# Kernel tuning notes

Hardware: AMD Instinct MI355X
Metric: run time of the kernel (lower is better)

Reference implementation:

```python
import jax, jax.numpy as jnp
import numpy as np
from jax.scipy.special import logsumexp

N, T, F, S, L = 16, 800, 90, 128, 200
NEG = -1e30
DEN_SCALE = 1.0


def setup_inputs() -> dict:
    key = jax.random.key(0)
    ks = jax.random.split(key, 6)
    # nnet_output is the output of log_softmax (per the docstring)
    logits = jax.random.normal(ks[0], (N, T, F), dtype=jnp.float32)
    nnet_output = jax.nn.log_softmax(logits, axis=-1)
    seq_idx = jnp.arange(N, dtype=jnp.int32)
    starts = jnp.zeros((N,), dtype=jnp.int32)
    nframes = jax.random.randint(ks[1], (N,), T // 2, T + 1).astype(jnp.int32)
    supervision_segments = jnp.stack([seq_idx, starts, nframes], axis=1)
    # shared denominator graph: dense log transition weights + state phone labels
    den_trans = jax.random.normal(ks[2], (S, S), dtype=jnp.float32) - 2.0
    den_labels = jax.random.randint(ks[3], (S,), 0, F).astype(jnp.int32)
    # numerator linear-chain graphs: per-utterance phone label sequences
    num_labels = jax.random.randint(ks[4], (N, L), 0, F).astype(jnp.int32)
    num_lens = jax.random.randint(ks[5], (N,), L // 2, L + 1).astype(jnp.int32)
    return {
        'nnet_output': nnet_output,
        'supervision_segments': supervision_segments,
        'den_trans': den_trans,
        'den_labels': den_labels,
        'num_labels': num_labels,
        'num_lens': num_lens,
    }


def _mmi_tot_scores(nnet_output, num_frames, den_trans, den_labels, num_labels, num_lens):
    """Log-semiring forward scores: num - den_scale * den per utterance."""
    x = jnp.transpose(nnet_output, (1, 0, 2))  # [T, N, F]
    ts = jnp.arange(T)

    # ---- denominator: shared dense WFSA, forward algorithm ----
    def den_step(alpha, inp):
        x_t, t = inp  # x_t: [N, F]
        emit = x_t[:, den_labels]  # [N, S] gather of frame log-probs
        new = logsumexp(alpha[:, :, None] + den_trans[None, :, :], axis=1) + emit
        alpha = jnp.where((t < num_frames)[:, None], new, alpha)
        return alpha, None

    a0 = jnp.full((N, S), NEG, dtype=nnet_output.dtype).at[:, 0].set(0.0)
    den_alpha, _ = jax.lax.scan(den_step, a0, (x, ts))
    den_scores = logsumexp(den_alpha, axis=1)  # [N]

    # ---- numerator: per-utterance linear chain (self-loop or advance) ----
    def num_step(alpha, inp):
        x_t, t = inp
        emit = jnp.take_along_axis(x_t, num_labels, axis=1)  # [N, L]
        body = jnp.logaddexp(alpha[:, 1:], alpha[:, :L]) + emit
        new = jnp.concatenate(
            [jnp.full((N, 1), NEG, dtype=alpha.dtype), body], axis=1)
        alpha = jnp.where((t < num_frames)[:, None], new, alpha)
        return alpha, None

    b0 = jnp.full((N, L + 1), NEG, dtype=nnet_output.dtype).at[:, 0].set(0.0)
    num_alpha, _ = jax.lax.scan(num_step, b0, (x, ts))
    num_scores = jnp.take_along_axis(num_alpha, num_lens[:, None], axis=1)[:, 0]

    return num_scores - DEN_SCALE * den_scores


def reference(nnet_output, supervision_segments, den_trans, den_labels, num_labels, num_lens):
    num_frames = supervision_segments[:, 2]
    tot = _mmi_tot_scores(nnet_output, num_frames, den_trans, den_labels,
                          num_labels, num_lens)
    # drop sequences whose score diverged (mirrors get_tot_objf_and_num_frames)
    finite = jnp.isfinite(tot) & (tot > 0.5 * NEG)
    tot_score = jnp.sum(jnp.where(finite, tot, 0.0))
    tot_frames = jnp.sum(jnp.where(finite, num_frames, 0))
    all_frames = jnp.sum(num_frames)
    return tot_score, tot_frames, all_frames
```

## Files before the change

kernel.cpp:

```cpp
#include <hip/hip_runtime.h>
#include <math.h>

#define NB 16
#define TT 800
#define FF 90
#define SS 128
#define LL 200
#define NEGV (-1e30f)

#define DNODES 16
#define DNDRX 50
#define QNODES 32
#define QDRX 25
#define BROW 26
#define NEGH (-60000.0f)
#define RST 68
#define LN2F 0.69314718055994531f
#define LOG2E 1.4426950408889634f

typedef __attribute__((ext_vector_type(8))) short short8;
typedef __attribute__((ext_vector_type(4))) float float4v;

static __device__ __forceinline__ unsigned short f2bf(float x) {
    union { float f; unsigned u; } v; v.f = x;
    unsigned r = (v.u + 0x7FFFu + ((v.u >> 16) & 1u)) >> 16;
    return (unsigned short)r;
}
static __device__ __forceinline__ unsigned pack2bf_t(float a, float b) {
    return (__float_as_uint(a) >> 16) | (__float_as_uint(b) & 0xFFFF0000u);
}

__global__ __launch_bounds__(256) void mmi_prep(const float* __restrict__ trans,
                                                unsigned* __restrict__ AF) {
    const int idx = blockIdx.x * 256 + threadIdx.x;
    const int l  = idx & 63, fk = idx >> 6;
    const int mt = fk >> 2, kc = fk & 3;
    const int q  = l >> 4,  m15 = l & 15;
    unsigned wv[4];
    #pragma unroll
    for (int j2 = 0; j2 < 4; ++j2) {
        const float a = __expf(trans[(kc * 32 + q * 8 + 2 * j2    ) * SS + mt * 16 + m15]);
        const float b = __expf(trans[(kc * 32 + q * 8 + 2 * j2 + 1) * SS + mt * 16 + m15]);
        wv[j2] = (unsigned)f2bf(a) | ((unsigned)f2bf(b) << 16);
    }
    *(uint4*)(AF + 4 * idx) = make_uint4(wv[0], wv[1], wv[2], wv[3]);
}

__global__ __launch_bounds__(512, 2) void mmi_nodes(
    const float* __restrict__ x,
    const int*   __restrict__ sup,
    const float* __restrict__ trans,
    const int*   __restrict__ den_labels,
    const int*   __restrict__ num_labels,
    const unsigned* __restrict__ AF,
    unsigned*    __restrict__ Pout,
    float*       __restrict__ scales8,
    _Float16*    __restrict__ Bd)
{
    __shared__ __align__(16) unsigned char SMEM[60448];
    const int tid = threadIdx.x;

    if (blockIdx.x < NB * DNODES) {
        unsigned* Xs  = (unsigned*)SMEM;
        float* ptab   = (float*)(SMEM + 34816);

        const int bid = blockIdx.x;
        const int u  = bid >> 4;
        const int nd = bid & 15;
        const int t0 = nd * DNDRX;
        const int nf = sup[u * 3 + 2];
        unsigned* Pg = Pout + (size_t)bid * 8192;

        if (t0 >= nf) {
            #pragma unroll
            for (int k2 = 0; k2 < 16; ++k2) {
                const int ww = tid + k2 * 512;
                const int row = ww >> 6, colw = ww & 63;
                unsigned val = 0;
                if (row == 2 * colw)     val |= 0x3F80u;
                if (row == 2 * colw + 1) val |= 0x3F800000u;
                Pg[ww] = val;
            }
            if (tid < 8) scales8[bid * 8 + tid] = 0.0f;
            return;
        }

        const int w = tid >> 6, l = tid & 63;
        const int m15 = l & 15, q = l >> 4;

        for (int idx = tid; idx < DNDRX * SS; idx += 512) {
            const int tt = idx >> 7, d = idx & 127;
            const int fr = min(t0 + tt, TT - 1);
            ptab[idx] = __expf(x[((size_t)u * TT + fr) * FF + den_labels[d]]);
        }
        __syncthreads();

        unsigned* Xw = Xs + w * (16 * RST);
        {
            const float p0 = ptab[2 * l], p1 = ptab[2 * l + 1];
            #pragma unroll
            for (int k2 = 0; k2 < 16; ++k2) {
                const int R = w * 16 + k2;
                const float2 t2 = ((const float2*)trans)[R * 64 + l];
                Xw[k2 * RST + l] = pack2bf_t(__expf(t2.x) * p0, __expf(t2.y) * p1);
            }
        }

        short8 afrag[8][4];
        #pragma unroll
        for (int mt = 0; mt < 8; ++mt)
            #pragma unroll
            for (int kc = 0; kc < 4; ++kc)
                afrag[mt][kc] = *(const short8*)(AF + ((mt * 4 + kc) * 64 + l) * 4);

        const unsigned short* XwH = (const unsigned short*)Xw;
        const int kmax = min(DNDRX, nf - t0);
        int eacc = 0;
        float redmax = 1.0f;

        for (int k = 1; k < kmax; ++k) {
            float sc = 1.0f;
            if ((k & 3) == 0) {
                const float mm = fmaxf(redmax, 1e-37f);
                const int e = (int)((__float_as_uint(mm) >> 23) & 255u);
                sc = __uint_as_float((unsigned)(254 - e) << 23);
                eacc += (e - 127);
            }

            short8 bf[4];
            #pragma unroll
            for (int kc = 0; kc < 4; ++kc)
                bf[kc] = *(const short8*)(XwH + m15 * (2 * RST) + kc * 32 + q * 8);

            float4v acc[8];
            #pragma unroll
            for (int mt = 0; mt < 8; ++mt) {
                float4v z = {0.f, 0.f, 0.f, 0.f};
                acc[mt] = z;
            }
            #pragma unroll
            for (int kc = 0; kc < 4; ++kc)
                #pragma unroll
                for (int mt = 0; mt < 8; ++mt)
                    acc[mt] = __builtin_amdgcn_mfma_f32_16x16x32_bf16(
                        afrag[mt][kc], bf[kc], acc[mt], 0, 0, 0);

            const bool dmax = ((k & 3) == 3);
            float vmax = 0.0f;
            #pragma unroll
            for (int mt = 0; mt < 8; ++mt) {
                float4 pc = *(const float4*)(ptab + k * SS + mt * 16 + 4 * q);
                pc.x *= sc; pc.y *= sc; pc.z *= sc; pc.w *= sc;
                acc[mt][0] *= pc.x;
                acc[mt][1] *= pc.y;
                acc[mt][2] *= pc.z;
                acc[mt][3] *= pc.w;
                if (dmax)
                    vmax = fmaxf(vmax,
                        fmaxf(fmaxf(acc[mt][0], acc[mt][1]),
                              fmaxf(acc[mt][2], acc[mt][3])));
            }
            if (dmax) {
                #pragma unroll
                for (int off = 32; off >= 1; off >>= 1)
                    vmax = fmaxf(vmax, __shfl_xor(vmax, off, 64));
                redmax = vmax;
            }

            #pragma unroll
            for (int mt = 0; mt < 8; ++mt) {
                uint2 pk;
                pk.x = pack2bf_t(acc[mt][0], acc[mt][1]);
                pk.y = pack2bf_t(acc[mt][2], acc[mt][3]);
                *(uint2*)(Xw + m15 * RST + mt * 8 + 2 * q) = pk;
            }
        }

        #pragma unroll
        for (int k2 = 0; k2 < 16; ++k2)
            Pg[(w * 16 + k2) * 64 + l] = Xw[k2 * RST + l];
        if (l == 0) scales8[bid * 8 + w] = (float)eacc;
        return;
    }

    {
        float* est = (float*)SMEM;

        const int qb    = blockIdx.x - NB * DNODES;
        const int slot0 = qb * 2;
        const int u     = slot0 / QNODES;
        const int nd0   = slot0 - u * QNODES;
        const int nf    = sup[u * 3 + 2];
        const int* nlu  = num_labels + u * LL;

        for (int idx = tid; idx < 2 * QDRX * 200; idx += 512) {
            const int g   = idx / (QDRX * 200);
            const int rem = idx - g * (QDRX * 200);
            const int tt  = rem / 200;
            const int j   = rem - tt * 200;
            const int fr  = min((nd0 + g) * QDRX + tt, TT - 1);
            est[idx] = x[((size_t)u * TT + fr) * FF + nlu[j]] * LOG2E;
        }
        __syncthreads();

        const int g  = tid >> 8;
        const int c  = tid & 255;
        const int nd = nd0 + g;
        const int t0 = nd * QDRX;
        const int kmaxg = min(QDRX, max(nf - t0, 0));
        const float* eg = est + g * (QDRX * 200);

        float a[BROW];
        a[0] = 0.0f;
        #pragma unroll
        for (int d = 1; d < BROW; ++d) a[d] = NEGV;

        for (int t = 0; t < kmaxg; ++t) {
            const float* et = eg + t * 200;
            #pragma unroll
            for (int d = BROW - 1; d >= 1; --d) {
                const float e  = et[min(c + d - 1, 199)];
                const float aa = a[d], bb = a[d - 1];
                const float mx = fmaxf(aa, bb);
                const float dd = fminf(aa, bb) - mx;
                a[d] = e + mx +
                       __builtin_amdgcn_logf(1.0f + __builtin_amdgcn_exp2f(dd));
            }
            a[0] = (c == 0) ? NEGV : (et[min(c - 1, 199)] + a[0]);
        }

        if (c <= 200) {
            _Float16* Bg = Bd + (size_t)(slot0 + g) * 201 * BROW;
            #pragma unroll
            for (int d = 0; d < BROW; ++d) {
                const int r = c + d;
                if (r <= 200) Bg[r * BROW + d] = (_Float16)fmaxf(a[d], NEGH);
            }
            if (c < BROW - 1) {
                for (int kk = c + 1; kk < BROW; ++kk)
                    Bg[c * BROW + kk] = (_Float16)NEGH;
            }
        }
    }
}

__global__ __launch_bounds__(256) void mmi_chain(
    const unsigned short* __restrict__ Pmat,
    const _Float16* __restrict__ Bd,
    const float* __restrict__ scales8,
    const int* __restrict__ num_lens,
    float* __restrict__ dsc)
{
    __shared__ float sh_v[SS];
    __shared__ float sh_part[8 * SS];
    __shared__ float sh_red[2];
    __shared__ float ab[2][232];

    const int tid = threadIdx.x;

    if (blockIdx.x < NB) {
        const int u = blockIdx.x;
        const int gg = tid & 31, c = tid >> 5;
        const unsigned short* Pu = Pmat + (size_t)u * DNODES * 16384;

        if (tid < SS) sh_v[tid] = (tid == 0) ? 1.0f : 0.0f;
        int   e2acc = 0;
        float sscal = 0.0f;

        uint2 curm[16], nxt[16];
        #pragma unroll
        for (int j = 0; j < 16; ++j)
            curm[j] = *(const uint2*)(Pu + (16 * c + j) * SS + 4 * gg);
        __syncthreads();

        for (int i = 0; i < DNODES; ++i) {
            if (i + 1 < DNODES) {
                const unsigned short* Pn = Pu + (size_t)(i + 1) * 16384;
                #pragma unroll
                for (int j = 0; j < 16; ++j)
                    nxt[j] = *(const uint2*)(Pn + (16 * c + j) * SS + 4 * gg);
            }
            const float* s8 = scales8 + (size_t)(u * DNODES + i) * 8;
            float gmax = s8[0];
            #pragma unroll
            for (int g2 = 1; g2 < 8; ++g2) gmax = fmaxf(gmax, s8[g2]);
            const float fgr = __builtin_amdgcn_exp2f(s8[c] - gmax);
            sscal += gmax;

            const float4* av = (const float4*)(sh_v + 16 * c);
            float4 aa[4] = {av[0], av[1], av[2], av[3]};
            const float* as = (const float*)aa;
            float4 acc = make_float4(0.f, 0.f, 0.f, 0.f);
            #pragma unroll
            for (int j = 0; j < 16; ++j) {
                const float e0 = __uint_as_float(curm[j].x << 16);
                const float e1 = __uint_as_float(curm[j].x & 0xFFFF0000u);
                const float e2 = __uint_as_float(curm[j].y << 16);
                const float e3 = __uint_as_float(curm[j].y & 0xFFFF0000u);
                acc.x = fmaf(as[j], e0, acc.x);
                acc.y = fmaf(as[j], e1, acc.y);
                acc.z = fmaf(as[j], e2, acc.z);
                acc.w = fmaf(as[j], e3, acc.w);
            }
            acc.x *= fgr; acc.y *= fgr; acc.z *= fgr; acc.w *= fgr;
            *(float4*)(sh_part + c * SS + 4 * gg) = acc;
            __syncthreads();

            float v = 0.0f;
            if (tid < SS) {
                float y = 0.0f;
                #pragma unroll
                for (int cc = 0; cc < 8; ++cc) y += sh_part[cc * SS + tid];
                v = y;
                float m = v;
                #pragma unroll
                for (int off = 32; off >= 1; off >>= 1)
                    m = fmaxf(m, __shfl_xor(m, off, 64));
                if ((tid & 63) == 0) sh_red[tid >> 6] = m;
            }
            __syncthreads();
            if (tid < SS) {
                const float mm = fmaxf(fmaxf(sh_red[0], sh_red[1]), 1e-37f);
                const int e = (int)((__float_as_uint(mm) >> 23) & 255u);
                const float inv = __uint_as_float((unsigned)(254 - e) << 23);
                e2acc += (e - 127);
                sh_v[tid] = v * inv;
            }
            #pragma unroll
            for (int j = 0; j < 16; ++j) curm[j] = nxt[j];
            __syncthreads();
        }

        if (tid < SS) {
            float s = sh_v[tid];
            #pragma unroll
            for (int off = 32; off >= 1; off >>= 1)
                s += __shfl_xor(s, off, 64);
            if ((tid & 63) == 0) sh_red[tid >> 6] = s;
        }
        __syncthreads();
        if (tid == 0)
            dsc[u] = LN2F * ((float)e2acc + sscal) + __logf(sh_red[0] + sh_red[1]);
    } else {
        const int u = blockIdx.x - NB;
        const _Float16* Bu = Bd + (size_t)u * QNODES * 201 * BROW;
        const int r = tid;

        if (r < 232) { ab[0][r] = NEGV; ab[1][r] = NEGV; }
        float dv[BROW];
        if (r < 201) {
            #pragma unroll
            for (int k = 0; k < BROW; ++k) dv[k] = (float)Bu[r * BROW + k];
        }
        __syncthreads();
        if (r == 0) ab[0][QDRX] = 0.0f;
        __syncthreads();

        int cur = 0;
        for (int nd = 0; nd < QNODES; ++nd) {
            _Float16 nx[BROW];
            if (nd + 1 < QNODES && r < 201) {
                const _Float16* src = Bu + ((size_t)(nd + 1) * 201 + r) * BROW;
                #pragma unroll
                for (int k = 0; k < BROW; ++k) nx[k] = src[k];
            }
            float anew = NEGV;
            if (r < 201) {
                float tr[BROW];
                #pragma unroll
                for (int k = 0; k < BROW; ++k)
                    tr[k] = dv[k] + ab[cur][QDRX + r - k];
                float m = tr[0];
                #pragma unroll
                for (int k = 1; k < BROW; ++k) m = fmaxf(m, tr[k]);
                float s = 0.0f;
                #pragma unroll
                for (int k = 0; k < BROW; ++k)
                    s += __builtin_amdgcn_exp2f(tr[k] - m);
                anew = m + __builtin_amdgcn_logf(s);
            }
            if (r < 201) ab[cur ^ 1][QDRX + r] = anew;
            cur ^= 1;
            __syncthreads();
            if (r < 201) {
                #pragma unroll
                for (int k = 0; k < BROW; ++k) dv[k] = (float)nx[k];
            }
        }
        if (r == 0) dsc[NB + u] = ab[cur][QDRX + num_lens[u]] * LN2F;
    }
}

__global__ void mmi_finalize(const float* __restrict__ sc,
                             const int* __restrict__ sup,
                             float* __restrict__ out)
{
    const int tid = threadIdx.x;
    float tot_score = 0.0f, tot_frames = 0.0f, all_frames = 0.0f;
    if (tid < NB) {
        const float tot = sc[NB + tid] - sc[tid];
        const int nf = sup[tid * 3 + 2];
        const bool fin = isfinite(tot) && (tot > 0.5f * NEGV);
        tot_score  = fin ? tot : 0.0f;
        tot_frames = fin ? (float)nf : 0.0f;
        all_frames = (float)nf;
    }
    #pragma unroll
    for (int off = 32; off >= 1; off >>= 1) {
        tot_score  += __shfl_xor(tot_score, off, 64);
        tot_frames += __shfl_xor(tot_frames, off, 64);
        all_frames += __shfl_xor(all_frames, off, 64);
    }
    if (tid == 0) {
        out[0] = tot_score;
        out[1] = tot_frames;
        out[2] = all_frames;
    }
}

#define XBF (16 * FF)
__global__ __launch_bounds__(256) void mmi_forward_fb(
    const float* __restrict__ x, const int* __restrict__ sup,
    const float* __restrict__ trans, const int* __restrict__ den_labels,
    const int* __restrict__ num_labels, const int* __restrict__ num_lens,
    float* __restrict__ ws)
{
    const int tid = threadIdx.x;
    if (blockIdx.x < NB) {
        __shared__ float sh_v[SS];
        __shared__ float sh_part[8 * SS];
        __shared__ float sh_red[4];
        __shared__ __align__(16) float xbuf[2][XBF];
        const int n = blockIdx.x, nf = sup[n * 3 + 2];
        const int g = tid & 31, c = tid >> 5;
        float4 e[16];
        #pragma unroll
        for (int j = 0; j < 16; ++j) {
            const float4 t4 = *(const float4*)(trans + (size_t)(16 * c + j) * SS + 4 * g);
            e[j] = make_float4(__expf(t4.x), __expf(t4.y), __expf(t4.z), __expf(t4.w));
        }
        const int lab = (tid < SS) ? den_labels[tid & (SS - 1)] : 0;
        const float* xb = x + (size_t)n * TT * FF;
        {
            const float4* s0 = (const float4*)xb;
            float4 p0 = s0[tid]; float4 p1; if (tid < 104) p1 = s0[256 + tid];
            float4* d0 = (float4*)xbuf[0];
            d0[tid] = p0; if (tid < 104) d0[256 + tid] = p1;
        }
        if (tid < SS) sh_v[tid] = (tid == 0) ? 1.0f : 0.0f;
        float logM = 0.0f, v = 0.0f, pe = 0.0f;
        float4 pf0, pf1;
        __syncthreads();
        for (int t = 0; t < nf; ++t) {
            const int b = t >> 4;
            if (tid < SS) pe = __expf(xbuf[b & 1][(t & 15) * FF + lab]);
            float4 aa[4];
            { const float4* av = (const float4*)(sh_v + 16 * c);
              aa[0] = av[0]; aa[1] = av[1]; aa[2] = av[2]; aa[3] = av[3]; }
            const float* as = (const float*)aa;
            float4 acc = make_float4(0.f, 0.f, 0.f, 0.f);
            #pragma unroll
            for (int j = 0; j < 16; ++j) {
                acc.x = fmaf(as[j], e[j].x, acc.x); acc.y = fmaf(as[j], e[j].y, acc.y);
                acc.z = fmaf(as[j], e[j].z, acc.z); acc.w = fmaf(as[j], e[j].w, acc.w);
            }
            *(float4*)(sh_part + c * SS + 4 * g) = acc;
            if ((t & 15) == 8) {
                const int tn = (b + 1) * 16;
                if (tn < nf) {
                    const float4* s = (const float4*)(xb + (size_t)tn * FF);
                    pf0 = s[tid]; if (tid < 104) pf1 = s[256 + tid];
                }
            }
            __syncthreads();
            const bool rs = ((t & 15) == 15);
            if (tid < SS) {
                float y = 0.0f;
                #pragma unroll
                for (int cc = 0; cc < 8; ++cc) y += sh_part[cc * SS + tid];
                v = y * pe;
                if (rs) {
                    float m = v;
                    #pragma unroll
                    for (int off = 32; off >= 1; off >>= 1)
                        m = fmaxf(m, __shfl_xor(m, off, 64));
                    if ((tid & 63) == 0) sh_red[tid >> 6] = m;
                }
            }
            if (rs) {
                const int tn = (b + 1) * 16;
                if (tn < nf) {
                    float4* dst = (float4*)xbuf[(b + 1) & 1];
                    dst[tid] = pf0; if (tid < 104) dst[256 + tid] = pf1;
                }
                __syncthreads();
                if (tid < SS) {
                    float mm = fmaxf(fmaxf(sh_red[0], sh_red[1]), 1e-37f);
                    v *= (1.0f / mm); logM += __logf(mm);
                }
            }
            if (tid < SS) sh_v[tid] = v;
            __syncthreads();
        }
        if (tid < SS) {
            float ssum = v;
            #pragma unroll
            for (int off = 32; off >= 1; off >>= 1) ssum += __shfl_xor(ssum, off, 64);
            if ((tid & 63) == 0) sh_red[2 + (tid >> 6)] = ssum;
        }
        __syncthreads();
        if (tid == 0) ws[n] = logM + __logf(sh_red[2] + sh_red[3]);
    } else {
        const int w = tid >> 6, l = tid & 63;
        const int n = (blockIdx.x - NB) * 4 + w;
        const int nf = sup[n * 3 + 2];
        const float* xb = x + (size_t)n * TT * FF;
        const int* nl = num_labels + n * LL;
        int li[4];
        #pragma unroll
        for (int k = 0; k < 4; ++k) li[k] = nl[min(4 * l + k, LL - 1)];
        float a4[4] = {NEGV, NEGV, NEGV, NEGV};
        float ea[4], eb[4];
        #pragma unroll
        for (int k = 0; k < 4; ++k) ea[k] = xb[li[k]];
        { const float* xr = xb + (size_t)min(1, nf - 1) * FF;
          #pragma unroll
          for (int k = 0; k < 4; ++k) eb[k] = xr[li[k]]; }
        auto step = [&](float (&ee)[4], int t) {
            float left = __shfl_up(a4[3], 1, 64);
            if (l == 0) left = (t == 0) ? 0.0f : NEGV;
            float prev = left;
            #pragma unroll
            for (int k = 0; k < 4; ++k) {
                const float a = a4[k], b = prev;
                const float mx = fmaxf(a, b), mn = fminf(a, b);
                const float nv = mx + __logf(1.0f + __expf(mn - mx)) + ee[k];
                prev = a4[k]; a4[k] = nv;
            }
            const int t2 = min(t + 2, nf - 1);
            const float* xr = xb + (size_t)t2 * FF;
            #pragma unroll
            for (int k = 0; k < 4; ++k) ee[k] = xr[li[k]];
        };
        int t = 0;
        while (t < nf) { step(ea, t); ++t; if (t >= nf) break; step(eb, t); ++t; }
        const int idx = num_lens[n] - 1;
        if ((idx >> 2) == l) {
            const int kk = idx & 3;
            float vv = (kk == 0) ? a4[0] : (kk == 1) ? a4[1] : (kk == 2) ? a4[2] : a4[3];
            ws[NB + n] = vv;
        }
    }
}

extern "C" void kernel_launch(void* const* d_in, const int* in_sizes, int n_in,
                              void* d_out, int out_size, void* d_ws, size_t ws_size,
                              hipStream_t stream) {
    const float* x          = (const float*)d_in[0];
    const int*   sup        = (const int*)d_in[1];
    const float* trans      = (const float*)d_in[2];
    const int*   den_labels = (const int*)d_in[3];
    const int*   num_labels = (const int*)d_in[4];
    const int*   num_lens   = (const int*)d_in[5];
    float* out = (float*)d_out;

    const size_t PBYTES = (size_t)NB * DNODES * 32768;
    const size_t BBYTES = (size_t)NB * QNODES * 201 * BROW * 2;
    const size_t SCB    = (size_t)NB * DNODES * 8 * sizeof(float);
    const size_t SOFF   = PBYTES + BBYTES;
    const size_t AOFF   = SOFF + SCB + 64 * sizeof(float);
    const size_t NEEDED = AOFF + 2048 * 16;

    if (ws_size >= NEEDED) {
        unsigned*  Pout    = (unsigned*)d_ws;
        _Float16*  Bd      = (_Float16*)((char*)d_ws + PBYTES);
        float*     scales8 = (float*)((char*)d_ws + SOFF);
        float*     scores  = scales8 + NB * DNODES * 8;
        unsigned*  AF      = (unsigned*)((char*)d_ws + AOFF);
        mmi_prep<<<dim3(8), dim3(256), 0, stream>>>(trans, AF);
        mmi_nodes<<<dim3(512), dim3(512), 0, stream>>>(
            x, sup, trans, den_labels, num_labels, AF, Pout, scales8, Bd);
        mmi_chain<<<dim3(2 * NB), dim3(256), 0, stream>>>(
            (const unsigned short*)d_ws, Bd, scales8, num_lens, scores);
        mmi_finalize<<<dim3(1), dim3(64), 0, stream>>>(scores, sup, out);
    } else {
        float* ws = (float*)d_ws;
        mmi_forward_fb<<<dim3(20), dim3(256), 0, stream>>>(
            x, sup, trans, den_labels, num_labels, num_lens, ws);
        mmi_finalize<<<dim3(1), dim3(64), 0, stream>>>(ws, sup, out);
    }
}
```

Before: 188.1 us.

## Fuse prep, node, chain and finalize kernels via last-block atomic counters

Merges the four launches into one kernel. Each block now builds the bf16 transition fragments itself in shared memory, and per-utterance atomic counters let the last node block of each utterance run the chain reduction. A final counter then lets one block do the finalize. This removes three kernel launches and the gaps between them, in exchange for redundant fragment setup in every block, a memset launch, and serialized chain work inside the tail blocks. The bf16 pack is also switched to a byte-permute instruction, and the emission table gets padded rows.

Measured after the change: 359.8 us. +91.3%, slower.

```diff
diff --git a/kernel.cpp b/kernel.cpp
--- a/kernel.cpp
+++ b/kernel.cpp
@@ -15,6 +15,7 @@
 #define BROW 26
 #define NEGH (-60000.0f)
 #define RST 68
+#define EPAD 228
 #define LN2F 0.69314718055994531f
 #define LOG2E 1.4426950408889634f
 
@@ -26,46 +27,33 @@
     unsigned r = (v.u + 0x7FFFu + ((v.u >> 16) & 1u)) >> 16;
     return (unsigned short)r;
 }
-static __device__ __forceinline__ unsigned pack2bf_t(float a, float b) {
-    return (__float_as_uint(a) >> 16) | (__float_as_uint(b) & 0xFFFF0000u);
+static __device__ __forceinline__ unsigned packperm(float a, float b) {
+    return __builtin_amdgcn_perm(__float_as_uint(b), __float_as_uint(a),
+                                 0x07060302u);
 }
 
-__global__ __launch_bounds__(256) void mmi_prep(const float* __restrict__ trans,
-                                                unsigned* __restrict__ AF) {
-    const int idx = blockIdx.x * 256 + threadIdx.x;
-    const int l  = idx & 63, fk = idx >> 6;
-    const int mt = fk >> 2, kc = fk & 3;
-    const int q  = l >> 4,  m15 = l & 15;
-    unsigned wv[4];
-    #pragma unroll
-    for (int j2 = 0; j2 < 4; ++j2) {
-        const float a = __expf(trans[(kc * 32 + q * 8 + 2 * j2    ) * SS + mt * 16 + m15]);
-        const float b = __expf(trans[(kc * 32 + q * 8 + 2 * j2 + 1) * SS + mt * 16 + m15]);
-        wv[j2] = (unsigned)f2bf(a) | ((unsigned)f2bf(b) << 16);
-    }
-    *(uint4*)(AF + 4 * idx) = make_uint4(wv[0], wv[1], wv[2], wv[3]);
-}
-
-__global__ __launch_bounds__(512, 2) void mmi_nodes(
+__global__ __launch_bounds__(512, 2) void mmi_all(
     const float* __restrict__ x,
     const int*   __restrict__ sup,
     const float* __restrict__ trans,
     const int*   __restrict__ den_labels,
     const int*   __restrict__ num_labels,
-    const unsigned* __restrict__ AF,
+    const int*   __restrict__ num_lens,
     unsigned*    __restrict__ Pout,
     float*       __restrict__ scales8,
-    _Float16*    __restrict__ Bd)
+    _Float16*    __restrict__ Bd,
+    float*       __restrict__ dsc,
+    int*         __restrict__ ctr,
+    float*       __restrict__ out)
 {
     __shared__ __align__(16) unsigned char SMEM[60448];
+    __shared__ int sflag;
     const int tid = threadIdx.x;
+    int u;
 
     if (blockIdx.x < NB * DNODES) {
-        unsigned* Xs  = (unsigned*)SMEM;
-        float* ptab   = (float*)(SMEM + 34816);
-
         const int bid = blockIdx.x;
-        const int u  = bid >> 4;
+        u = bid >> 4;
         const int nd = bid & 15;
         const int t0 = nd * DNDRX;
         const int nf = sup[u * 3 + 2];
@@ -82,312 +70,376 @@
                 Pg[ww] = val;
             }
             if (tid < 8) scales8[bid * 8 + tid] = 0.0f;
-            return;
-        }
-
-        const int w = tid >> 6, l = tid & 63;
-        const int m15 = l & 15, q = l >> 4;
-
-        for (int idx = tid; idx < DNDRX * SS; idx += 512) {
-            const int tt = idx >> 7, d = idx & 127;
-            const int fr = min(t0 + tt, TT - 1);
-            ptab[idx] = __expf(x[((size_t)u * TT + fr) * FF + den_labels[d]]);
-        }
+        } else {
+            unsigned* AFs = (unsigned*)SMEM;
+            const int w = tid >> 6, l = tid & 63;
+            const int m15 = l & 15, q = l >> 4;
+
+            #pragma unroll
+            for (int i = 0; i < 16; ++i) {
+                const int wi = tid + i * 512;
+                const int f  = wi >> 2, j2 = wi & 3;
+                const int fl = f & 63, kc = (f >> 6) & 3, mt = f >> 8;
+                const int col = mt * 16 + (fl & 15);
+                const int krow = kc * 32 + (fl >> 4) * 8 + 2 * j2;
+                const float a = __expf(trans[(krow    ) * SS + col]);
+                const float b = __expf(trans[(krow + 1) * SS + col]);
+                AFs[wi] = (unsigned)f2bf(a) | ((unsigned)f2bf(b) << 16);
+            }
+            __syncthreads();
+            short8 afrag[8][4];
+            #pragma unroll
+            for (int mt = 0; mt < 8; ++mt)
+                #pragma unroll
+                for (int kc = 0; kc < 4; ++kc)
+                    afrag[mt][kc] =
+                        *(const short8*)(AFs + ((mt * 4 + kc) * 64 + l) * 4);
+            __syncthreads();
+
+            unsigned* Xs  = (unsigned*)SMEM;
+            float* ptab   = (float*)(SMEM + 34816);
+
+            for (int idx = tid; idx < DNDRX * SS; idx += 512) {
+                const int tt = idx >> 7, d = idx & 127;
+                const int fr = min(t0 + tt, TT - 1);
+                ptab[idx] = __expf(x[((size_t)u * TT + fr) * FF + den_labels[d]]);
+            }
+            __syncthreads();
+
+            unsigned* Xw = Xs + w * (16 * RST);
+            {
+                const float p0 = ptab[2 * l], p1 = ptab[2 * l + 1];
+                #pragma unroll
+                for (int k2 = 0; k2 < 16; ++k2) {
+                    const int R = w * 16 + k2;
+                    const float2 t2 = ((const float2*)trans)[R * 64 + l];
+                    Xw[k2 * RST + l] = packperm(__expf(t2.x) * p0,
+                                                __expf(t2.y) * p1);
+                }
+            }
+
+            const unsigned short* XwH = (const unsigned short*)Xw;
+            const int kmax = min(DNDRX, nf - t0);
+            int eacc = 0;
+            float redmax = 1.0f;
+
+            for (int k = 1; k < kmax; ++k) {
+                const bool dosc = ((k & 3) == 0);
+                float sc = 1.0f;
+                if (dosc) {
+                    const float mm = fmaxf(redmax, 1e-37f);
+                    const int e = (int)((__float_as_uint(mm) >> 23) & 255u);
+                    sc = __uint_as_float((unsigned)(254 - e) << 23);
+                    eacc += (e - 127);
+                }
+
+                short8 bf[4];
+                #pragma unroll
+                for (int kc = 0; kc < 4; ++kc)
+                    bf[kc] = *(const short8*)(XwH + m15 * (2 * RST) +
+                                              kc * 32 + q * 8);
+
+                float4v acc[8];
+                #pragma unroll
+                for (int mt = 0; mt < 8; ++mt) {
+                    float4v z = {0.f, 0.f, 0.f, 0.f};
+                    acc[mt] = z;
+                }
+                #pragma unroll
+                for (int kc = 0; kc < 4; ++kc)
+                    #pragma unroll
+                    for (int mt = 0; mt < 8; ++mt)
+                        acc[mt] = __builtin_amdgcn_mfma_f32_16x16x32_bf16(
+                            afrag[mt][kc], bf[kc], acc[mt], 0, 0, 0);
+
+                const bool dmax = ((k & 3) == 3);
+                float vmax = 0.0f;
+                #pragma unroll
+                for (int mt = 0; mt < 8; ++mt) {
+                    float4 pc = *(const float4*)(ptab + k * SS + mt * 16 + 4 * q);
+                    if (dosc) { pc.x *= sc; pc.y *= sc; pc.z *= sc; pc.w *= sc; }
+                    acc[mt][0] *= pc.x;
+                    acc[mt][1] *= pc.y;
+                    acc[mt][2] *= pc.z;
+                    acc[mt][3] *= pc.w;
+                    if (dmax)
+                        vmax = fmaxf(vmax,
+                            fmaxf(fmaxf(acc[mt][0], acc[mt][1]),
+                                  fmaxf(acc[mt][2], acc[mt][3])));
+                }
+                if (dmax) {
+                    #pragma unroll
+                    for (int off = 32; off >= 1; off >>= 1)
+                        vmax = fmaxf(vmax, __shfl_xor(vmax, off, 64));
+                    redmax = vmax;
+                }
+
+                #pragma unroll
+                for (int mt = 0; mt < 8; ++mt) {
+                    uint2 pk;
+                    pk.x = packperm(acc[mt][0], acc[mt][1]);
+                    pk.y = packperm(acc[mt][2], acc[mt][3]);
+                    *(uint2*)(Xw + m15 * RST + mt * 8 + 2 * q) = pk;
+                }
+            }
+
+            #pragma unroll
+            for (int k2 = 0; k2 < 16; ++k2)
+                Pg[(w * 16 + k2) * 64 + l] = Xw[k2 * RST + l];
+            if (l == 0) scales8[bid * 8 + w] = (float)eacc;
+        }
+
+        __threadfence();
+        if (tid == 0) sflag = (atomicAdd(&ctr[u], 1) == DNODES - 1);
         __syncthreads();
-
-        unsigned* Xw = Xs + w * (16 * RST);
+        if (!sflag) return;
         {
-            const float p0 = ptab[2 * l], p1 = ptab[2 * l + 1];
-            #pragma unroll
-            for (int k2 = 0; k2 < 16; ++k2) {
-                const int R = w * 16 + k2;
-                const float2 t2 = ((const float2*)trans)[R * 64 + l];
-                Xw[k2 * RST + l] = pack2bf_t(__expf(t2.x) * p0, __expf(t2.y) * p1);
-            }
-        }
-
-        short8 afrag[8][4];
-        #pragma unroll
-        for (int mt = 0; mt < 8; ++mt)
-            #pragma unroll
-            for (int kc = 0; kc < 4; ++kc)
-                afrag[mt][kc] = *(const short8*)(AF + ((mt * 4 + kc) * 64 + l) * 4);
-
-        const unsigned short* XwH = (const unsigned short*)Xw;
-        const int kmax = min(DNDRX, nf - t0);
-        int eacc = 0;
-        float redmax = 1.0f;
-
-        for (int k = 1; k < kmax; ++k) {
-            float sc = 1.0f;
-            if ((k & 3) == 0) {
-                const float mm = fmaxf(redmax, 1e-37f);
-                const int e = (int)((__float_as_uint(mm) >> 23) & 255u);
-                sc = __uint_as_float((unsigned)(254 - e) << 23);
-                eacc += (e - 127);
-            }
-
-            short8 bf[4];
-            #pragma unroll
-            for (int kc = 0; kc < 4; ++kc)
-                bf[kc] = *(const short8*)(XwH + m15 * (2 * RST) + kc * 32 + q * 8);
-
-            float4v acc[8];
-            #pragma unroll
-            for (int mt = 0; mt < 8; ++mt) {
-                float4v z = {0.f, 0.f, 0.f, 0.f};
-                acc[mt] = z;
-            }
-            #pragma unroll
-            for (int kc = 0; kc < 4; ++kc)
-                #pragma unroll
-                for (int mt = 0; mt < 8; ++mt)
-                    acc[mt] = __builtin_amdgcn_mfma_f32_16x16x32_bf16(
-                        afrag[mt][kc], bf[kc], acc[mt], 0, 0, 0);
-
-            const bool dmax = ((k & 3) == 3);
-            float vmax = 0.0f;
-            #pragma unroll
-            for (int mt = 0; mt < 8; ++mt) {
-                float4 pc = *(const float4*)(ptab + k * SS + mt * 16 + 4 * q);
-                pc.x *= sc; pc.y *= sc; pc.z *= sc; pc.w *= sc;
-                acc[mt][0] *= pc.x;
-                acc[mt][1] *= pc.y;
-                acc[mt][2] *= pc.z;
-                acc[mt][3] *= pc.w;
-                if (dmax)
-                    vmax = fmaxf(vmax,
-                        fmaxf(fmaxf(acc[mt][0], acc[mt][1]),
-                              fmaxf(acc[mt][2], acc[mt][3])));
-            }
-            if (dmax) {
+            float* sh_v    = (float*)SMEM;
+            float* sh_part = (float*)(SMEM + 512);
+            float* sh_red  = (float*)(SMEM + 4608);
+            __syncthreads();
+
+            const bool act = tid < 256;
+            const int gg = tid & 31, c = tid >> 5;
+            const unsigned short* Pu =
+                (const unsigned short*)(Pout + (size_t)u * DNODES * 8192);
+
+            if (tid < SS) sh_v[tid] = (tid == 0) ? 1.0f : 0.0f;
+            int   e2acc = 0;
+            float sscal = 0.0f;
+
+            uint2 curm[16], nxt[16];
+            if (act) {
+                #pragma unroll
+                for (int j = 0; j < 16; ++j)
+                    curm[j] = *(const uint2*)(Pu + (16 * c + j) * SS + 4 * gg);
+            }
+            __syncthreads();
+
+            for (int i = 0; i < DNODES; ++i) {
+                if (act && i + 1 < DNODES) {
+                    const unsigned short* Pn = Pu + (size_t)(i + 1) * 16384;
+                    #pragma unroll
+                    for (int j = 0; j < 16; ++j)
+                        nxt[j] = *(const uint2*)(Pn + (16 * c + j) * SS + 4 * gg);
+                }
+                float fgr = 0.0f;
+                if (act) {
+                    const float* s8 = scales8 + (size_t)(u * DNODES + i) * 8;
+                    float gmax = s8[0];
+                    #pragma unroll
+                    for (int g2 = 1; g2 < 8; ++g2) gmax = fmaxf(gmax, s8[g2]);
+                    fgr = __builtin_amdgcn_exp2f(s8[c & 7] - gmax);
+                    sscal += gmax;
+                }
+                if (act) {
+                    const float4* av = (const float4*)(sh_v + 16 * c);
+                    float4 aa[4] = {av[0], av[1], av[2], av[3]};
+                    const float* as = (const float*)aa;
+                    float4 acc = make_float4(0.f, 0.f, 0.f, 0.f);
+                    #pragma unroll
+                    for (int j = 0; j < 16; ++j) {
+                        const float e0 = __uint_as_float(curm[j].x << 16);
+                        const float e1 = __uint_as_float(curm[j].x & 0xFFFF0000u);
+                        const float e2 = __uint_as_float(curm[j].y << 16);
+                        const float e3 = __uint_as_float(curm[j].y & 0xFFFF0000u);
+                        acc.x = fmaf(as[j], e0, acc.x);
+                        acc.y = fmaf(as[j], e1, acc.y);
+                        acc.z = fmaf(as[j], e2, acc.z);
+                        acc.w = fmaf(as[j], e3, acc.w);
+                    }
+                    acc.x *= fgr; acc.y *= fgr; acc.z *= fgr; acc.w *= fgr;
+                    *(float4*)(sh_part + c * SS + 4 * gg) = acc;
+                }
+                __syncthreads();
+
+                float v = 0.0f;
+                if (tid < SS) {
+                    float y = 0.0f;
+                    #pragma unroll
+                    for (int cc = 0; cc < 8; ++cc) y += sh_part[cc * SS + tid];
+                    v = y;
+                    float m = v;
+                    #pragma unroll
+                    for (int off = 32; off >= 1; off >>= 1)
+                        m = fmaxf(m, __shfl_xor(m, off, 64));
+                    if ((tid & 63) == 0) sh_red[tid >> 6] = m;
+                }
+                __syncthreads();
+                if (tid < SS) {
+                    const float mm = fmaxf(fmaxf(sh_red[0], sh_red[1]), 1e-37f);
+                    const int e = (int)((__float_as_uint(mm) >> 23) & 255u);
+                    const float inv = __uint_as_float((unsigned)(254 - e) << 23);
+                    e2acc += (e - 127);
+                    sh_v[tid] = v * inv;
+                }
+                if (act) {
+                    #pragma unroll
+                    for (int j = 0; j < 16; ++j) curm[j] = nxt[j];
+                }
+                __syncthreads();
+            }
+
+            if (tid < SS) {
+                float s = sh_v[tid];
                 #pragma unroll
                 for (int off = 32; off >= 1; off >>= 1)
-                    vmax = fmaxf(vmax, __shfl_xor(vmax, off, 64));
-                redmax = vmax;
-            }
-
-            #pragma unroll
-            for (int mt = 0; mt < 8; ++mt) {
-                uint2 pk;
-                pk.x = pack2bf_t(acc[mt][0], acc[mt][1]);
-                pk.y = pack2bf_t(acc[mt][2], acc[mt][3]);
-                *(uint2*)(Xw + m15 * RST + mt * 8 + 2 * q) = pk;
-            }
-        }
-
-        #pragma unroll
-        for (int k2 = 0; k2 < 16; ++k2)
-            Pg[(w * 16 + k2) * 64 + l] = Xw[k2 * RST + l];
-        if (l == 0) scales8[bid * 8 + w] = (float)eacc;
-        return;
-    }
-
-    {
-        float* est = (float*)SMEM;
+                    s += __shfl_xor(s, off, 64);
+                if ((tid & 63) == 0) sh_red[tid >> 6] = s;
+            }
+            __syncthreads();
+            if (tid == 0)
+                dsc[u] = LN2F * ((float)e2acc + sscal) +
+                         __logf(sh_red[0] + sh_red[1]);
+        }
+    } else {
+        float* est = (float*)(SMEM + 16);
 
         const int qb    = blockIdx.x - NB * DNODES;
         const int slot0 = qb * 2;
-        const int u     = slot0 / QNODES;
+        u = slot0 / QNODES;
         const int nd0   = slot0 - u * QNODES;
         const int nf    = sup[u * 3 + 2];
         const int* nlu  = num_labels + u * LL;
 
-        for (int idx = tid; idx < 2 * QDRX * 200; idx += 512) {
-            const int g   = idx / (QDRX * 200);
-            const int rem = idx - g * (QDRX * 200);
-            const int tt  = rem / 200;
-            const int j   = rem - tt * 200;
+        for (int idx = tid; idx < 2 * QDRX * EPAD; idx += 512) {
+            const int g   = idx / (QDRX * EPAD);
+            const int rem = idx - g * (QDRX * EPAD);
+            const int tt  = rem / EPAD;
+            const int j   = rem - tt * EPAD;
+            const int jj  = min(j, 199);
             const int fr  = min((nd0 + g) * QDRX + tt, TT - 1);
-            est[idx] = x[((size_t)u * TT + fr) * FF + nlu[j]] * LOG2E;
+            est[idx] = x[((size_t)u * TT + fr) * FF + nlu[jj]] * LOG2E;
         }
         __syncthreads();
 
-        const int g  = tid >> 8;
-        const int c  = tid & 255;
-        const int nd = nd0 + g;
-        const int t0 = nd * QDRX;
-        const int kmaxg = min(QDRX, max(nf - t0, 0));
-        const float* eg = est + g * (QDRX * 200);
-
-        float a[BROW];
-        a[0] = 0.0f;
+        {
+            const int g  = tid >> 8;
+            const int c  = tid & 255;
+            const int nd = nd0 + g;
+            const int t0 = nd * QDRX;
+            const int kmaxg = min(QDRX, max(nf - t0, 0));
+            const float* eg = est + g * (QDRX * EPAD);
+
+            float a[BROW];
+            a[0] = 0.0f;
+            #pragma unroll
+            for (int d = 1; d < BROW; ++d) a[d] = NEGV;
+
+            const float* etc = eg + (c - 1);
+            for (int t = 0; t < kmaxg; ++t, etc += EPAD) {
+                const int tc = t + 1;
+                #pragma unroll
+                for (int d = BROW - 1; d >= 1; --d) {
+                    if (d <= tc) {
+                        const float e  = etc[d];
+                        const float aa = a[d], bb = a[d - 1];
+                        const float mx = fmaxf(aa, bb);
+                        const float dd = fminf(aa, bb) - mx;
+                        a[d] = e + mx +
+                            __builtin_amdgcn_logf(
+                                1.0f + __builtin_amdgcn_exp2f(dd));
+                    }
+                }
+                a[0] = (c == 0) ? NEGV : (etc[0] + a[0]);
+            }
+
+            if (c <= 200) {
+                _Float16* Bg = Bd + (size_t)(slot0 + g) * 201 * BROW;
+                #pragma unroll
+                for (int d = 0; d < BROW; ++d) {
+                    const int r = c + d;
+                    if (r <= 200) Bg[r * BROW + d] = (_Float16)fmaxf(a[d], NEGH);
+                }
+                if (c < BROW - 1) {
+                    for (int kk = c + 1; kk < BROW; ++kk)
+                        Bg[c * BROW + kk] = (_Float16)NEGH;
+                }
+            }
+        }
+
+        __threadfence();
+        if (tid == 0) sflag = (atomicAdd(&ctr[NB + u], 1) == QNODES / 2 - 1);
+        __syncthreads();
+        if (!sflag) return;
+        {
+            float (*ab)[232] = (float (*)[232])SMEM;
+            __syncthreads();
+
+            const _Float16* Bu = Bd + (size_t)u * QNODES * 201 * BROW;
+            const int r = tid;
+
+            if (r < 232) { ab[0][r] = NEGV; ab[1][r] = NEGV; }
+            float dv[BROW];
+            if (r < 201) {
+                #pragma unroll
+                for (int k = 0; k < BROW; ++k) dv[k] = (float)Bu[r * BROW + k];
+            }
+            __syncthreads();
+            if (r == 0) ab[0][QDRX] = 0.0f;
+            __syncthreads();
+
+            int cur = 0;
+            for (int nd = 0; nd < QNODES; ++nd) {
+                _Float16 nx[BROW];
+                if (nd + 1 < QNODES && r < 201) {
+                    const _Float16* src = Bu + ((size_t)(nd + 1) * 201 + r) * BROW;
+                    #pragma unroll
+                    for (int k = 0; k < BROW; ++k) nx[k] = src[k];
+                }
+                float anew = NEGV;
+                if (r < 201) {
+                    float tr[BROW];
+                    #pragma unroll
+                    for (int k = 0; k < BROW; ++k)
+                        tr[k] = dv[k] + ab[cur][QDRX + r - k];
+                    float m = tr[0];
+                    #pragma unroll
+                    for (int k = 1; k < BROW; ++k) m = fmaxf(m, tr[k]);
+                    float s = 0.0f;
+                    #pragma unroll
+                    for (int k = 0; k < BROW; ++k)
+                        s += __builtin_amdgcn_exp2f(tr[k] - m);
+                    anew = m + __builtin_amdgcn_logf(s);
+                }
+                if (r < 201) ab[cur ^ 1][QDRX + r] = anew;
+                cur ^= 1;
+                __syncthreads();
+                if (r < 201) {
+                    #pragma unroll
+                    for (int k = 0; k < BROW; ++k) dv[k] = (float)nx[k];
+                }
+            }
+            if (r == 0) dsc[NB + u] = ab[cur][QDRX + num_lens[u]] * LN2F;
+        }
+    }
+
+    __threadfence();
+    if (tid == 0) sflag = (atomicAdd(&ctr[2 * NB], 1) == 2 * NB - 1);
+    __syncthreads();
+    if (!sflag) return;
+    __threadfence();
+    if (tid < 64) {
+        float tot_score = 0.0f, tot_frames = 0.0f, all_frames = 0.0f;
+        if (tid < NB) {
+            const float tot = dsc[NB + tid] - dsc[tid];
+            const int nf = sup[tid * 3 + 2];
+            const bool fin = isfinite(tot) && (tot > 0.5f * NEGV);
+            tot_score  = fin ? tot : 0.0f;
+            tot_frames = fin ? (float)nf : 0.0f;
+            all_frames = (float)nf;
+        }
         #pragma unroll
-        for (int d = 1; d < BROW; ++d) a[d] = NEGV;
-
-        for (int t = 0; t < kmaxg; ++t) {
-            const float* et = eg + t * 200;
-            #pragma unroll
-            for (int d = BROW - 1; d >= 1; --d) {
-                const float e  = et[min(c + d - 1, 199)];
-                const float aa = a[d], bb = a[d - 1];
-                const float mx = fmaxf(aa, bb);
-                const float dd = fminf(aa, bb) - mx;
-                a[d] = e + mx +
-                       __builtin_amdgcn_logf(1.0f + __builtin_amdgcn_exp2f(dd));
-            }
-            a[0] = (c == 0) ? NEGV : (et[min(c - 1, 199)] + a[0]);
-        }
-
-        if (c <= 200) {
-            _Float16* Bg = Bd + (size_t)(slot0 + g) * 201 * BROW;
-            #pragma unroll
-            for (int d = 0; d < BROW; ++d) {
-                const int r = c + d;
-                if (r <= 200) Bg[r * BROW + d] = (_Float16)fmaxf(a[d], NEGH);
-            }
-            if (c < BROW - 1) {
-                for (int kk = c + 1; kk < BROW; ++kk)
-                    Bg[c * BROW + kk] = (_Float16)NEGH;
-            }
-        }
-    }
-}
-
-__global__ __launch_bounds__(256) void mmi_chain(
-    const unsigned short* __restrict__ Pmat,
-    const _Float16* __restrict__ Bd,
-    const float* __restrict__ scales8,
-    const int* __restrict__ num_lens,
-    float* __restrict__ dsc)
-{
-    __shared__ float sh_v[SS];
-    __shared__ float sh_part[8 * SS];
-    __shared__ float sh_red[2];
-    __shared__ float ab[2][232];
-
-    const int tid = threadIdx.x;
-
-    if (blockIdx.x < NB) {
-        const int u = blockIdx.x;
-        const int gg = tid & 31, c = tid >> 5;
-        const unsigned short* Pu = Pmat + (size_t)u * DNODES * 16384;
-
-        if (tid < SS) sh_v[tid] = (tid == 0) ? 1.0f : 0.0f;
-        int   e2acc = 0;
-        float sscal = 0.0f;
-
-        uint2 curm[16], nxt[16];
-        #pragma unroll
-        for (int j = 0; j < 16; ++j)
-            curm[j] = *(const uint2*)(Pu + (16 * c + j) * SS + 4 * gg);
-        __syncthreads();
-
-        for (int i = 0; i < DNODES; ++i) {
-            if (i + 1 < DNODES) {
-                const unsigned short* Pn = Pu + (size_t)(i + 1) * 16384;
-                #pragma unroll
-                for (int j = 0; j < 16; ++j)
-                    nxt[j] = *(const uint2*)(Pn + (16 * c + j) * SS + 4 * gg);
-            }
-            const float* s8 = scales8 + (size_t)(u * DNODES + i) * 8;
-            float gmax = s8[0];
-            #pragma unroll
-            for (int g2 = 1; g2 < 8; ++g2) gmax = fmaxf(gmax, s8[g2]);
-            const float fgr = __builtin_amdgcn_exp2f(s8[c] - gmax);
-            sscal += gmax;
-
-            const float4* av = (const float4*)(sh_v + 16 * c);
-            float4 aa[4] = {av[0], av[1], av[2], av[3]};
-            const float* as = (const float*)aa;
-            float4 acc = make_float4(0.f, 0.f, 0.f, 0.f);
-            #pragma unroll
-            for (int j = 0; j < 16; ++j) {
-                const float e0 = __uint_as_float(curm[j].x << 16);
-                const float e1 = __uint_as_float(curm[j].x & 0xFFFF0000u);
-                const float e2 = __uint_as_float(curm[j].y << 16);
-                const float e3 = __uint_as_float(curm[j].y & 0xFFFF0000u);
-                acc.x = fmaf(as[j], e0, acc.x);
-                acc.y = fmaf(as[j], e1, acc.y);
-                acc.z = fmaf(as[j], e2, acc.z);
-                acc.w = fmaf(as[j], e3, acc.w);
-            }
-            acc.x *= fgr; acc.y *= fgr; acc.z *= fgr; acc.w *= fgr;
-            *(float4*)(sh_part + c * SS + 4 * gg) = acc;
-            __syncthreads();
-
-            float v = 0.0f;
-            if (tid < SS) {
-                float y = 0.0f;
-                #pragma unroll
-                for (int cc = 0; cc < 8; ++cc) y += sh_part[cc * SS + tid];
-                v = y;
-                float m = v;
-                #pragma unroll
-                for (int off = 32; off >= 1; off >>= 1)
-                    m = fmaxf(m, __shfl_xor(m, off, 64));
-                if ((tid & 63) == 0) sh_red[tid >> 6] = m;
-            }
-            __syncthreads();
-            if (tid < SS) {
-                const float mm = fmaxf(fmaxf(sh_red[0], sh_red[1]), 1e-37f);
-                const int e = (int)((__float_as_uint(mm) >> 23) & 255u);
-                const float inv = __uint_as_float((unsigned)(254 - e) << 23);
-                e2acc += (e - 127);
-                sh_v[tid] = v * inv;
-            }
-            #pragma unroll
-            for (int j = 0; j < 16; ++j) curm[j] = nxt[j];
-            __syncthreads();
-        }
-
-        if (tid < SS) {
-            float s = sh_v[tid];
-            #pragma unroll
-            for (int off = 32; off >= 1; off >>= 1)
-                s += __shfl_xor(s, off, 64);
-            if ((tid & 63) == 0) sh_red[tid >> 6] = s;
-        }
-        __syncthreads();
-        if (tid == 0)
-            dsc[u] = LN2F * ((float)e2acc + sscal) + __logf(sh_red[0] + sh_red[1]);
-    } else {
-        const int u = blockIdx.x - NB;
-        const _Float16* Bu = Bd + (size_t)u * QNODES * 201 * BROW;
-        const int r = tid;
-
-        if (r < 232) { ab[0][r] = NEGV; ab[1][r] = NEGV; }
-        float dv[BROW];
-        if (r < 201) {
-            #pragma unroll
-            for (int k = 0; k < BROW; ++k) dv[k] = (float)Bu[r * BROW + k];
-        }
-        __syncthreads();
-        if (r == 0) ab[0][QDRX] = 0.0f;
-        __syncthreads();
-
-        int cur = 0;
-        for (int nd = 0; nd < QNODES; ++nd) {
-            _Float16 nx[BROW];
-            if (nd + 1 < QNODES && r < 201) {
-                const _Float16* src = Bu + ((size_t)(nd + 1) * 201 + r) * BROW;
-                #pragma unroll
-                for (int k = 0; k < BROW; ++k) nx[k] = src[k];
-            }
-            float anew = NEGV;
-            if (r < 201) {
-                float tr[BROW];
-                #pragma unroll
-                for (int k = 0; k < BROW; ++k)
-                    tr[k] = dv[k] + ab[cur][QDRX + r - k];
-                float m = tr[0];
-                #pragma unroll
-                for (int k = 1; k < BROW; ++k) m = fmaxf(m, tr[k]);
-                float s = 0.0f;
-                #pragma unroll
-                for (int k = 0; k < BROW; ++k)
-                    s += __builtin_amdgcn_exp2f(tr[k] - m);
-                anew = m + __builtin_amdgcn_logf(s);
-            }
-            if (r < 201) ab[cur ^ 1][QDRX + r] = anew;
-            cur ^= 1;
-            __syncthreads();
-            if (r < 201) {
-                #pragma unroll
-                for (int k = 0; k < BROW; ++k) dv[k] = (float)nx[k];
-            }
-        }
-        if (r == 0) dsc[NB + u] = ab[cur][QDRX + num_lens[u]] * LN2F;
+        for (int off = 32; off >= 1; off >>= 1) {
+            tot_score  += __shfl_xor(tot_score, off, 64);
+            tot_frames += __shfl_xor(tot_frames, off, 64);
+            all_frames += __shfl_xor(all_frames, off, 64);
+        }
+        if (tid == 0) {
+            out[0] = tot_score;
+            out[1] = tot_frames;
+            out[2] = all_frames;
+        }
     }
 }
 
@@ -568,21 +620,20 @@
     const size_t BBYTES = (size_t)NB * QNODES * 201 * BROW * 2;
     const size_t SCB    = (size_t)NB * DNODES * 8 * sizeof(float);
     const size_t SOFF   = PBYTES + BBYTES;
-    const size_t AOFF   = SOFF + SCB + 64 * sizeof(float);
-    const size_t NEEDED = AOFF + 2048 * 16;
+    const size_t DOFF   = SOFF + SCB;
+    const size_t COFF   = DOFF + 256;
+    const size_t NEEDED = COFF + 256;
 
     if (ws_size >= NEEDED) {
         unsigned*  Pout    = (unsigned*)d_ws;
         _Float16*  Bd      = (_Float16*)((char*)d_ws + PBYTES);
         float*     scales8 = (float*)((char*)d_ws + SOFF);
-        float*     scores  = scales8 + NB * DNODES * 8;
-        unsigned*  AF      = (unsigned*)((char*)d_ws + AOFF);
-        mmi_prep<<<dim3(8), dim3(256), 0, stream>>>(trans, AF);
-        mmi_nodes<<<dim3(512), dim3(512), 0, stream>>>(
-            x, sup, trans, den_labels, num_labels, AF, Pout, scales8, Bd);
-        mmi_chain<<<dim3(2 * NB), dim3(256), 0, stream>>>(
-            (const unsigned short*)d_ws, Bd, scales8, num_lens, scores);
-        mmi_finalize<<<dim3(1), dim3(64), 0, stream>>>(scores, sup, out);
+        float*     dsc     = (float*)((char*)d_ws + DOFF);
+        int*       ctr     = (int*)((char*)d_ws + COFF);
+        hipMemsetAsync(ctr, 0, 256, stream);
+        mmi_all<<<dim3(512), dim3(512), 0, stream>>>(
+            x, sup, trans, den_labels, num_labels, num_lens,
+            Pout, scales8, Bd, dsc, ctr, out);
     } else {
         float* ws = (float*)d_ws;
         mmi_forward_fb<<<dim3(20), dim3(256), 0, stream>>>(
```

## Halve den ptab in two phases, pad numerator emission rows, skip unreachable diagonals

Applied to the files above, without the earlier changes.

The denominator node path now computes the emission-probability table in two 25-frame phases instead of one 50-frame table. This shrinks shared memory from about 60KB to 47KB, presumably to allow more resident blocks, at the cost of an extra barrier and a mid-loop reload. The numerator path pads emission rows to 228 so per-element min() clamps disappear, and it skips diagonals d greater than t+1, which cannot yet hold finite values. The bf16 packing now uses a byte-permute instruction, and the scale multiply is applied only on rescale steps.

Result: faster. 183.0 us (-2.7%).

```diff
diff --git a/kernel.cpp b/kernel.cpp
--- a/kernel.cpp
+++ b/kernel.cpp
@@ -10,11 +10,13 @@
 
 #define DNODES 16
 #define DNDRX 50
+#define PTROWS 25
 #define QNODES 32
 #define QDRX 25
 #define BROW 26
 #define NEGH (-60000.0f)
 #define RST 68
+#define EPAD 228
 #define LN2F 0.69314718055994531f
 #define LOG2E 1.4426950408889634f
 
@@ -26,8 +28,9 @@
     unsigned r = (v.u + 0x7FFFu + ((v.u >> 16) & 1u)) >> 16;
     return (unsigned short)r;
 }
-static __device__ __forceinline__ unsigned pack2bf_t(float a, float b) {
-    return (__float_as_uint(a) >> 16) | (__float_as_uint(b) & 0xFFFF0000u);
+static __device__ __forceinline__ unsigned packperm(float a, float b) {
+    return __builtin_amdgcn_perm(__float_as_uint(b), __float_as_uint(a),
+                                 0x07060302u);
 }
 
 __global__ __launch_bounds__(256) void mmi_prep(const float* __restrict__ trans,
@@ -57,7 +60,7 @@
     float*       __restrict__ scales8,
     _Float16*    __restrict__ Bd)
 {
-    __shared__ __align__(16) unsigned char SMEM[60448];
+    __shared__ __align__(16) unsigned char SMEM[47616];
     const int tid = threadIdx.x;
 
     if (blockIdx.x < NB * DNODES) {
@@ -88,7 +91,7 @@
         const int w = tid >> 6, l = tid & 63;
         const int m15 = l & 15, q = l >> 4;
 
-        for (int idx = tid; idx < DNDRX * SS; idx += 512) {
+        for (int idx = tid; idx < PTROWS * SS; idx += 512) {
             const int tt = idx >> 7, d = idx & 127;
             const int fr = min(t0 + tt, TT - 1);
             ptab[idx] = __expf(x[((size_t)u * TT + fr) * FF + den_labels[d]]);
@@ -102,7 +105,8 @@
             for (int k2 = 0; k2 < 16; ++k2) {
                 const int R = w * 16 + k2;
                 const float2 t2 = ((const float2*)trans)[R * 64 + l];
-                Xw[k2 * RST + l] = pack2bf_t(__expf(t2.x) * p0, __expf(t2.y) * p1);
+                Xw[k2 * RST + l] = packperm(__expf(t2.x) * p0,
+                                            __expf(t2.y) * p1);
             }
         }
 
@@ -118,62 +122,82 @@
         int eacc = 0;
         float redmax = 1.0f;
 
-        for (int k = 1; k < kmax; ++k) {
-            float sc = 1.0f;
-            if ((k & 3) == 0) {
-                const float mm = fmaxf(redmax, 1e-37f);
-                const int e = (int)((__float_as_uint(mm) >> 23) & 255u);
-                sc = __uint_as_float((unsigned)(254 - e) << 23);
-                eacc += (e - 127);
-            }
-
-            short8 bf[4];
-            #pragma unroll
-            for (int kc = 0; kc < 4; ++kc)
-                bf[kc] = *(const short8*)(XwH + m15 * (2 * RST) + kc * 32 + q * 8);
-
-            float4v acc[8];
-            #pragma unroll
-            for (int mt = 0; mt < 8; ++mt) {
-                float4v z = {0.f, 0.f, 0.f, 0.f};
-                acc[mt] = z;
-            }
-            #pragma unroll
-            for (int kc = 0; kc < 4; ++kc)
-                #pragma unroll
-                for (int mt = 0; mt < 8; ++mt)
-                    acc[mt] = __builtin_amdgcn_mfma_f32_16x16x32_bf16(
-                        afrag[mt][kc], bf[kc], acc[mt], 0, 0, 0);
-
-            const bool dmax = ((k & 3) == 3);
-            float vmax = 0.0f;
-            #pragma unroll
-            for (int mt = 0; mt < 8; ++mt) {
-                float4 pc = *(const float4*)(ptab + k * SS + mt * 16 + 4 * q);
-                pc.x *= sc; pc.y *= sc; pc.z *= sc; pc.w *= sc;
-                acc[mt][0] *= pc.x;
-                acc[mt][1] *= pc.y;
-                acc[mt][2] *= pc.z;
-                acc[mt][3] *= pc.w;
-                if (dmax)
-                    vmax = fmaxf(vmax,
-                        fmaxf(fmaxf(acc[mt][0], acc[mt][1]),
-                              fmaxf(acc[mt][2], acc[mt][3])));
-            }
-            if (dmax) {
-                #pragma unroll
-                for (int off = 32; off >= 1; off >>= 1)
-                    vmax = fmaxf(vmax, __shfl_xor(vmax, off, 64));
-                redmax = vmax;
-            }
-
-            #pragma unroll
-            for (int mt = 0; mt < 8; ++mt) {
-                uint2 pk;
-                pk.x = pack2bf_t(acc[mt][0], acc[mt][1]);
-                pk.y = pack2bf_t(acc[mt][2], acc[mt][3]);
-                *(uint2*)(Xw + m15 * RST + mt * 8 + 2 * q) = pk;
-            }
+        int kbeg = 1;
+        for (int ph = 0; ph < 2 && kbeg < kmax; ++ph) {
+            const int kend = min(kmax, PTROWS * (ph + 1));
+            const int kofs = ph * PTROWS;
+            if (ph == 1) {
+                __syncthreads();
+                for (int idx = tid; idx < PTROWS * SS; idx += 512) {
+                    const int tt = PTROWS + (idx >> 7), d = idx & 127;
+                    const int fr = min(t0 + tt, TT - 1);
+                    ptab[idx] = __expf(x[((size_t)u * TT + fr) * FF +
+                                         den_labels[d]]);
+                }
+                __syncthreads();
+            }
+
+            for (int k = kbeg; k < kend; ++k) {
+                const bool dosc = ((k & 3) == 0);
+                float sc = 1.0f;
+                if (dosc) {
+                    const float mm = fmaxf(redmax, 1e-37f);
+                    const int e = (int)((__float_as_uint(mm) >> 23) & 255u);
+                    sc = __uint_as_float((unsigned)(254 - e) << 23);
+                    eacc += (e - 127);
+                }
+
+                short8 bf[4];
+                #pragma unroll
+                for (int kc = 0; kc < 4; ++kc)
+                    bf[kc] = *(const short8*)(XwH + m15 * (2 * RST) +
+                                              kc * 32 + q * 8);
+
+                float4v acc[8];
+                #pragma unroll
+                for (int mt = 0; mt < 8; ++mt) {
+                    float4v z = {0.f, 0.f, 0.f, 0.f};
+                    acc[mt] = z;
+                }
+                #pragma unroll
+                for (int kc = 0; kc < 4; ++kc)
+                    #pragma unroll
+                    for (int mt = 0; mt < 8; ++mt)
+                        acc[mt] = __builtin_amdgcn_mfma_f32_16x16x32_bf16(
+                            afrag[mt][kc], bf[kc], acc[mt], 0, 0, 0);
+
+                const bool dmax = ((k & 3) == 3);
+                float vmax = 0.0f;
+                #pragma unroll
+                for (int mt = 0; mt < 8; ++mt) {
+                    float4 pc = *(const float4*)(ptab + (k - kofs) * SS +
+                                                 mt * 16 + 4 * q);
+                    if (dosc) { pc.x *= sc; pc.y *= sc; pc.z *= sc; pc.w *= sc; }
+                    acc[mt][0] *= pc.x;
+                    acc[mt][1] *= pc.y;
+                    acc[mt][2] *= pc.z;
+                    acc[mt][3] *= pc.w;
+                    if (dmax)
+                        vmax = fmaxf(vmax,
+                            fmaxf(fmaxf(acc[mt][0], acc[mt][1]),
+                                  fmaxf(acc[mt][2], acc[mt][3])));
+                }
+                if (dmax) {
+                    #pragma unroll
+                    for (int off = 32; off >= 1; off >>= 1)
+                        vmax = fmaxf(vmax, __shfl_xor(vmax, off, 64));
+                    redmax = vmax;
+                }
+
+                #pragma unroll
+                for (int mt = 0; mt < 8; ++mt) {
+                    uint2 pk;
+                    pk.x = packperm(acc[mt][0], acc[mt][1]);
+                    pk.y = packperm(acc[mt][2], acc[mt][3]);
+                    *(uint2*)(Xw + m15 * RST + mt * 8 + 2 * q) = pk;
+                }
+            }
+            kbeg = kend;
         }
 
         #pragma unroll
@@ -184,7 +208,7 @@
     }
 
     {
-        float* est = (float*)SMEM;
+        float* est = (float*)(SMEM + 16);
 
         const int qb    = blockIdx.x - NB * DNODES;
         const int slot0 = qb * 2;
@@ -193,13 +217,14 @@
         const int nf    = sup[u * 3 + 2];
         const int* nlu  = num_labels + u * LL;
 
-        for (int idx = tid; idx < 2 * QDRX * 200; idx += 512) {
-            const int g   = idx / (QDRX * 200);
-            const int rem = idx - g * (QDRX * 200);
-            const int tt  = rem / 200;
-            const int j   = rem - tt * 200;
+        for (int idx = tid; idx < 2 * QDRX * EPAD; idx += 512) {
+            const int g   = idx / (QDRX * EPAD);
+            const int rem = idx - g * (QDRX * EPAD);
+            const int tt  = rem / EPAD;
+            const int j   = rem - tt * EPAD;
+            const int jj  = min(j, 199);
             const int fr  = min((nd0 + g) * QDRX + tt, TT - 1);
-            est[idx] = x[((size_t)u * TT + fr) * FF + nlu[j]] * LOG2E;
+            est[idx] = x[((size_t)u * TT + fr) * FF + nlu[jj]] * LOG2E;
         }
         __syncthreads();
 
@@ -208,25 +233,29 @@
         const int nd = nd0 + g;
         const int t0 = nd * QDRX;
         const int kmaxg = min(QDRX, max(nf - t0, 0));
-        const float* eg = est + g * (QDRX * 200);
+        const float* eg = est + g * (QDRX * EPAD);
 
         float a[BROW];
         a[0] = 0.0f;
         #pragma unroll
         for (int d = 1; d < BROW; ++d) a[d] = NEGV;
 
-        for (int t = 0; t < kmaxg; ++t) {
-            const float* et = eg + t * 200;
+        const float* etc = eg + (c - 1);
+        for (int t = 0; t < kmaxg; ++t, etc += EPAD) {
+            const int tc = t + 1;
             #pragma unroll
             for (int d = BROW - 1; d >= 1; --d) {
-                const float e  = et[min(c + d - 1, 199)];
-                const float aa = a[d], bb = a[d - 1];
-                const float mx = fmaxf(aa, bb);
-                const float dd = fminf(aa, bb) - mx;
-                a[d] = e + mx +
-                       __builtin_amdgcn_logf(1.0f + __builtin_amdgcn_exp2f(dd));
-            }
-            a[0] = (c == 0) ? NEGV : (et[min(c - 1, 199)] + a[0]);
+                if (d <= tc) {
+                    const float e  = etc[d];
+                    const float aa = a[d], bb = a[d - 1];
+                    const float mx = fmaxf(aa, bb);
+                    const float dd = fminf(aa, bb) - mx;
+                    a[d] = e + mx +
+                           __builtin_amdgcn_logf(
+                               1.0f + __builtin_amdgcn_exp2f(dd));
+                }
+            }
+            a[0] = (c == 0) ? NEGV : (etc[0] + a[0]);
         }
 
         if (c <= 200) {
```
